# Performance work log

Hardware: AMD Instinct MI355X
Metric: run time of the kernel (lower is better)

## Reference

```python
import jax, jax.numpy as jnp
import numpy as np

GS = 8      # grid_size
NH = 8      # num_heads
DM = 256    # hidden_dim / d_model
B, W, H = 4, 256, 256


def setup_inputs() -> dict:
    key = jax.random.key(0)
    ks = jax.random.split(key, 5)
    s = 0.02
    return {
        "x": jax.random.normal(ks[0], (B, DM, W, H), dtype=jnp.float32),
        "Wq": jax.random.normal(ks[1], (DM, DM), dtype=jnp.float32) * s,
        "bq": jnp.zeros((DM,), dtype=jnp.float32),
        "Wk": jax.random.normal(ks[2], (DM, DM), dtype=jnp.float32) * s,
        "bk": jnp.zeros((DM,), dtype=jnp.float32),
        "Wv": jax.random.normal(ks[3], (DM, DM), dtype=jnp.float32) * s,
        "bv": jnp.zeros((DM,), dtype=jnp.float32),
        "Wo": jax.random.normal(ks[4], (DM, DM), dtype=jnp.float32) * s,
        "bo": jnp.zeros((DM,), dtype=jnp.float32),
    }


def reference(x, Wq, bq, Wk, bk, Wv, bv, Wo, bo):
    b, d, w, h = x.shape
    gw, gh = w // GS, h // GS
    n = gw * gh               # num grid cells
    L = GS * GS               # tokens per cell
    dh = d // NH

    # query: avg-pool each grid cell -> (b*n, 1, d)
    q = x.reshape(b, d, gw, GS, gh, GS).mean(axis=(3, 5))      # (b, d, gw, gh)
    q = q.reshape(b, d, n).transpose(0, 2, 1).reshape(b * n, 1, d)

    # K/V: per-cell patch tokens, (b*n, L, d); matches torch unfold layout
    kv = x.transpose(0, 2, 3, 1)                                # (b, w, h, d)
    kv = kv.reshape(b, gw, GS, gh, GS, d)
    kv = kv.transpose(0, 1, 3, 2, 4, 5).reshape(b * n, L, d)

    # multi-head cross-attention (standard: q/k/v/out linear + softmax)
    qp = (q @ Wq.T + bq).reshape(b * n, 1, NH, dh).transpose(0, 2, 1, 3)   # (bn, H, 1, dh)
    kp = (kv @ Wk.T + bk).reshape(b * n, L, NH, dh).transpose(0, 2, 1, 3)  # (bn, H, L, dh)
    vp = (kv @ Wv.T + bv).reshape(b * n, L, NH, dh).transpose(0, 2, 1, 3)

    scores = jnp.einsum("bhqd,bhkd->bhqk", qp, kp) / jnp.sqrt(jnp.float32(dh))
    attn = jax.nn.softmax(scores, axis=-1)                      # (bn, H, 1, L)
    ctx = jnp.einsum("bhqk,bhkd->bhqd", attn, vp)               # (bn, H, 1, dh)
    ctx = ctx.transpose(0, 2, 1, 3).reshape(b * n, 1, d)
    attn_out = ctx @ Wo.T + bo                                  # (bn, 1, d)

    out = q + attn_out
    return out.reshape(b, n, d)
```

## Files before the change

kernel.cpp:

```cpp
#include <hip/hip_runtime.h>
#include <hip/hip_bf16.h>


#define NCELL 4096

typedef float f32x4 __attribute__((ext_vector_type(4)));
typedef short s16x8 __attribute__((ext_vector_type(8)));

#define OFF_NT 0u
#define OFF_BE 262144u
#define OFF_S 1310976u
#define OFF_WQB 5505280u
#define OFF_WKB 5538048u

__device__ __forceinline__ unsigned short bfrnd(float f) {
  unsigned u = __float_as_uint(f);
  u += 0x7fffu + ((u >> 16) & 1u);
  return (unsigned short)(u >> 16);
}
__device__ __forceinline__ float bflo(unsigned u) { return __uint_as_float(u << 16); }
__device__ __forceinline__ float bfhi(unsigned u) { return __uint_as_float(u & 0xffff0000u); }

__global__ __launch_bounds__(256) void k_cvt(const float* __restrict__ Wq, const float* __restrict__ Wk,
                                             unsigned short* __restrict__ WQB, unsigned short* __restrict__ WKB) {
  const int i = blockIdx.x * 256 + threadIdx.x;
  {
    const float4 v = *reinterpret_cast<const float4*>(Wq + i * 4);
    const unsigned lo = (unsigned)bfrnd(v.x) | ((unsigned)bfrnd(v.y) << 16);
    const unsigned hi = (unsigned)bfrnd(v.z) | ((unsigned)bfrnd(v.w) << 16);
    *reinterpret_cast<uint2*>(WQB + i * 4) = make_uint2(lo, hi);
  }
  {
    const float4 v = *reinterpret_cast<const float4*>(Wk + i * 4);
    const unsigned lo = (unsigned)bfrnd(v.x) | ((unsigned)bfrnd(v.y) << 16);
    const unsigned hi = (unsigned)bfrnd(v.z) | ((unsigned)bfrnd(v.w) << 16);
    *reinterpret_cast<uint2*>(WKB + i * 4) = make_uint2(lo, hi);
  }
}

__global__ __launch_bounds__(256) void k_nt(const float* __restrict__ Wv, const float* __restrict__ Wo,
                                            unsigned short* __restrict__ NT) {
  __shared__ float wo_s[32];
  const int n = blockIdx.x >> 3, h = blockIdx.x & 7;
  const int j = threadIdx.x;
  if (threadIdx.x < 32) wo_s[threadIdx.x] = Wo[n * 256 + h * 32 + threadIdx.x];
  __syncthreads();
  float acc = 0.f;
#pragma unroll
  for (int i = 0; i < 32; ++i) acc += Wv[(h * 32 + i) * 256 + j] * wo_s[i];
  NT[(size_t)n * 2048 + h * 256 + j] = bfrnd(acc);
}

__global__ __launch_bounds__(256) void k_beff(const float* __restrict__ bo, const float* __restrict__ bv,
                                              const float* __restrict__ Wo, float* __restrict__ BE) {
  const int w = threadIdx.x >> 6, l = threadIdx.x & 63;
  const int k = blockIdx.x * 4 + w;
  float acc = 0.f;
#pragma unroll
  for (int c = 0; c < 4; ++c) acc += bv[l + 64 * c] * Wo[k * 256 + l + 64 * c];
#pragma unroll
  for (int mk = 32; mk >= 1; mk >>= 1) acc += __shfl_xor(acc, mk);
  if (l == 0) BE[k] = acc + bo[k];
}

__global__ __launch_bounds__(256, 3) void k_cell(
    const float* __restrict__ x,
    const unsigned short* __restrict__ WQB, const float* __restrict__ bq,
    const unsigned short* __restrict__ WKB, const float* __restrict__ bk,
    const float* __restrict__ BE,
    float* __restrict__ out, unsigned short* __restrict__ Sg) {
  __shared__ __align__(16) unsigned short xb[256 * 72];
  __shared__ __align__(16) float q_s[256];
  __shared__ __align__(16) float qp_s[256];
  __shared__ __align__(16) unsigned short r_bf[8 * 264];
  __shared__ __align__(16) float R1[2304];
  __shared__ float off_s[8];

  const int tid = threadIdx.x;
  const int cell = ((blockIdx.x & 7) << 9) | (blockIdx.x >> 3);
  const int b = cell >> 10, cw = (cell >> 5) & 31, ch = cell & 31;
  const float* xp = x + (size_t)b * 16777216 + (size_t)cw * 2048 + (size_t)ch * 8;

  const int i_row = (tid >> 1) & 7, half = tid & 1, d0 = tid >> 4;
  const float* tb = xp + (size_t)d0 * 65536 + i_row * 256 + half * 4;
  float4 v[16];
#pragma unroll
  for (int it = 0; it < 16; ++it)
    v[it] = *reinterpret_cast<const float4*>(tb + (size_t)it * 1048576);
  const int t0 = i_row * 8 + half * 4;
#pragma unroll
  for (int it = 0; it < 16; ++it) {
    const int d = it * 16 + d0;
    const unsigned lo = (unsigned)bfrnd(v[it].x) | ((unsigned)bfrnd(v[it].y) << 16);
    const unsigned hi = (unsigned)bfrnd(v[it].z) | ((unsigned)bfrnd(v[it].w) << 16);
    *reinterpret_cast<uint2*>(&xb[d * 72 + t0]) = make_uint2(lo, hi);
    float ps = (v[it].x + v[it].y) + (v[it].z + v[it].w);
    ps += __shfl_xor(ps, 1);
    ps += __shfl_xor(ps, 2);
    ps += __shfl_xor(ps, 4);
    ps += __shfl_xor(ps, 8);
    if ((tid & 15) == 0) q_s[d] = ps * (1.0f / 64.0f);
  }
  __syncthreads();

  out[(size_t)cell * 256 + tid] = q_s[tid] + BE[tid];

  {
    const int io = tid >> 5, jl = tid & 31;
    float qr[8];
    *reinterpret_cast<float4*>(qr) = *reinterpret_cast<const float4*>(&q_s[jl * 8]);
    *reinterpret_cast<float4*>(qr + 4) = *reinterpret_cast<const float4*>(&q_s[jl * 8 + 4]);
#pragma unroll
    for (int rb = 0; rb < 8; ++rb) {
      float acc[4];
#pragma unroll
      for (int rr = 0; rr < 4; ++rr) {
        const int i = (rb * 4 + rr) * 8 + io;
        const uint4 wv = *reinterpret_cast<const uint4*>(WQB + i * 256 + jl * 8);
        acc[rr] = bflo(wv.x) * qr[0] + bfhi(wv.x) * qr[1] + bflo(wv.y) * qr[2] + bfhi(wv.y) * qr[3] +
                  bflo(wv.z) * qr[4] + bfhi(wv.z) * qr[5] + bflo(wv.w) * qr[6] + bfhi(wv.w) * qr[7];
      }
#pragma unroll
      for (int mk = 16; mk >= 1; mk >>= 1) {
#pragma unroll
        for (int rr = 0; rr < 4; ++rr) acc[rr] += __shfl_xor(acc[rr], mk);
      }
      if (jl == 0) {
#pragma unroll
        for (int rr = 0; rr < 4; ++rr) {
          const int i = (rb * 4 + rr) * 8 + io;
          qp_s[i] = (acc[rr] + bq[i]) * 0.17677669529663689f;
        }
      }
    }
  }
  __syncthreads();

  {
    const int hw = tid >> 6;
    const int j0 = (tid & 63) * 4;
#pragma unroll
    for (int hh = 0; hh < 2; ++hh) {
      const int h = hw * 2 + hh;
      float a0 = 0.f, a1 = 0.f, a2 = 0.f, a3 = 0.f;
#pragma unroll
      for (int i = 0; i < 32; ++i) {
        const float s = qp_s[h * 32 + i];
        const uint2 wv = *reinterpret_cast<const uint2*>(WKB + (h * 32 + i) * 256 + j0);
        a0 += s * bflo(wv.x);
        a1 += s * bfhi(wv.x);
        a2 += s * bflo(wv.y);
        a3 += s * bfhi(wv.y);
      }
      const unsigned lo = (unsigned)bfrnd(a0) | ((unsigned)bfrnd(a1) << 16);
      const unsigned hi = (unsigned)bfrnd(a2) | ((unsigned)bfrnd(a3) << 16);
      *reinterpret_cast<uint2*>(&r_bf[h * 264 + j0]) = make_uint2(lo, hi);
    }
    if (tid < 8) {
      float o = 0.f;
      for (int i = 0; i < 32; ++i) o += qp_s[tid * 32 + i] * bk[tid * 32 + i];
      off_s[tid] = o;
    }
  }
  __syncthreads();

  {
    const int t = tid & 63, p = tid >> 6;
    float xr[64];
#pragma unroll
    for (int dd = 0; dd < 64; ++dd) {
      const unsigned vv = xb[(p * 64 + dd) * 72 + t];
      xr[dd] = __uint_as_float(vv << 16);
    }
#pragma unroll
    for (int h = 0; h < 8; ++h) {
      float acc = 0.f;
#pragma unroll
      for (int dc = 0; dc < 8; ++dc) {
        const uint4 rv = *reinterpret_cast<const uint4*>(&r_bf[h * 264 + p * 64 + dc * 8]);
        acc += bflo(rv.x) * xr[dc * 8 + 0] + bfhi(rv.x) * xr[dc * 8 + 1] +
               bflo(rv.y) * xr[dc * 8 + 2] + bfhi(rv.y) * xr[dc * 8 + 3] +
               bflo(rv.z) * xr[dc * 8 + 4] + bfhi(rv.z) * xr[dc * 8 + 5] +
               bflo(rv.w) * xr[dc * 8 + 6] + bfhi(rv.w) * xr[dc * 8 + 7];
      }
      R1[p * 576 + t * 9 + h] = acc;
    }
  }
  __syncthreads();

  {
    const int w = tid >> 6, t = tid & 63;
    float av[2];
#pragma unroll
    for (int hi = 0; hi < 2; ++hi) {
      const int h = w + hi * 4;
      const float vv = R1[0 * 576 + t * 9 + h] + R1[1 * 576 + t * 9 + h] +
                       R1[2 * 576 + t * 9 + h] + R1[3 * 576 + t * 9 + h] + off_s[h];
      float m = vv;
#pragma unroll
      for (int mk = 32; mk >= 1; mk >>= 1) m = fmaxf(m, __shfl_xor(m, mk));
      const float e = __expf(vv - m);
      float s = e;
#pragma unroll
      for (int mk = 32; mk >= 1; mk >>= 1) s += __shfl_xor(s, mk);
      av[hi] = e / s;
    }
    __syncthreads();
    R1[t * 12 + w] = av[0];
    R1[t * 12 + w + 4] = av[1];
  }
  __syncthreads();

  {
    const int d = tid;
    float acc[8] = {0, 0, 0, 0, 0, 0, 0, 0};
#pragma unroll
    for (int tc = 0; tc < 8; ++tc) {
      const uint4 xv = *reinterpret_cast<const uint4*>(&xb[d * 72 + tc * 8]);
      const float xf[8] = {bflo(xv.x), bfhi(xv.x), bflo(xv.y), bfhi(xv.y),
                           bflo(xv.z), bfhi(xv.z), bflo(xv.w), bfhi(xv.w)};
#pragma unroll
      for (int k = 0; k < 8; ++k) {
        const int t = tc * 8 + k;
        const float4 aA = *reinterpret_cast<const float4*>(&R1[t * 12]);
        const float4 aB = *reinterpret_cast<const float4*>(&R1[t * 12 + 4]);
        acc[0] += aA.x * xf[k]; acc[1] += aA.y * xf[k];
        acc[2] += aA.z * xf[k]; acc[3] += aA.w * xf[k];
        acc[4] += aB.x * xf[k]; acc[5] += aB.y * xf[k];
        acc[6] += aB.z * xf[k]; acc[7] += aB.w * xf[k];
      }
    }
#pragma unroll
    for (int h = 0; h < 8; ++h)
      Sg[(size_t)cell * 2048 + h * 256 + d] = bfrnd(acc[h]);
  }
}

__global__ __launch_bounds__(256, 4) void k_out(
    const unsigned short* __restrict__ Sg, const unsigned short* __restrict__ NT,
    float* __restrict__ out) {
  __shared__ __align__(16) unsigned short As[64 * 72];
  __shared__ __align__(16) unsigned short Bs[64 * 72];
  const int tid = threadIdx.x;
  const int tile = blockIdx.x >> 2, ks = blockIdx.x & 3;
  const int m0 = (tile >> 2) * 64, n0 = (tile & 3) * 64;
  const int w = tid >> 6, l = tid & 63;
  const int wm = (w & 1) * 32, wn = (w >> 1) * 32;
  const int lr = l & 15, lq = l >> 4;

  f32x4 acc[2][2];
#pragma unroll
  for (int a = 0; a < 2; ++a)
#pragma unroll
    for (int c = 0; c < 2; ++c) acc[a][c] = (f32x4){0.f, 0.f, 0.f, 0.f};

  const int srow = tid >> 2, sseg = tid & 3;
  const size_t arow = (size_t)(m0 + srow) * 2048 + sseg * 16;
  const size_t brow = (size_t)(n0 + srow) * 2048 + sseg * 16;
  const int kbase = ks * 512;

  uint4 a0v = *reinterpret_cast<const uint4*>(&Sg[arow + kbase]);
  uint4 a1v = *reinterpret_cast<const uint4*>(&Sg[arow + kbase + 8]);
  uint4 b0v = *reinterpret_cast<const uint4*>(&NT[brow + kbase]);
  uint4 b1v = *reinterpret_cast<const uint4*>(&NT[brow + kbase + 8]);

  for (int kt = 0; kt < 8; ++kt) {
    __syncthreads();
    *reinterpret_cast<uint4*>(&As[srow * 72 + sseg * 16]) = a0v;
    *reinterpret_cast<uint4*>(&As[srow * 72 + sseg * 16 + 8]) = a1v;
    *reinterpret_cast<uint4*>(&Bs[srow * 72 + sseg * 16]) = b0v;
    *reinterpret_cast<uint4*>(&Bs[srow * 72 + sseg * 16 + 8]) = b1v;
    __syncthreads();
    if (kt < 7) {
      const int kn = kbase + (kt + 1) * 64;
      a0v = *reinterpret_cast<const uint4*>(&Sg[arow + kn]);
      a1v = *reinterpret_cast<const uint4*>(&Sg[arow + kn + 8]);
      b0v = *reinterpret_cast<const uint4*>(&NT[brow + kn]);
      b1v = *reinterpret_cast<const uint4*>(&NT[brow + kn + 8]);
    }
#pragma unroll
    for (int s = 0; s < 2; ++s) {
      s16x8 af[2], bfr[2];
#pragma unroll
      for (int a = 0; a < 2; ++a)
        af[a] = *reinterpret_cast<const s16x8*>(&As[(wm + a * 16 + lr) * 72 + s * 32 + lq * 8]);
#pragma unroll
      for (int c = 0; c < 2; ++c)
        bfr[c] = *reinterpret_cast<const s16x8*>(&Bs[(wn + c * 16 + lr) * 72 + s * 32 + lq * 8]);
#pragma unroll
      for (int a = 0; a < 2; ++a)
#pragma unroll
        for (int c = 0; c < 2; ++c)
          acc[a][c] = __builtin_amdgcn_mfma_f32_16x16x32_bf16(af[a], bfr[c], acc[a][c], 0, 0, 0);
    }
  }
#pragma unroll
  for (int a = 0; a < 2; ++a) {
#pragma unroll
    for (int c = 0; c < 2; ++c) {
      const int col = n0 + wn + c * 16 + lr;
#pragma unroll
      for (int rr = 0; rr < 4; ++rr) {
        const int row = m0 + wm + a * 16 + lq * 4 + rr;
        atomicAdd(&out[(size_t)row * 256 + col], acc[a][c][rr]);
      }
    }
  }
}

extern "C" void kernel_launch(void* const* d_in, const int* in_sizes, int n_in,
                              void* d_out, int out_size, void* d_ws, size_t ws_size,
                              hipStream_t stream) {
  const float* x = (const float*)d_in[0];
  const float* Wq = (const float*)d_in[1];
  const float* bq = (const float*)d_in[2];
  const float* Wk = (const float*)d_in[3];
  const float* bk = (const float*)d_in[4];
  const float* Wv = (const float*)d_in[5];
  const float* bv = (const float*)d_in[6];
  const float* Wo = (const float*)d_in[7];
  const float* bo = (const float*)d_in[8];
  float* ws = (float*)d_ws;
  unsigned short* NT = (unsigned short*)(ws + OFF_NT);
  float* BE = ws + OFF_BE;
  unsigned short* Sg = (unsigned short*)(ws + OFF_S);
  unsigned short* WQB = (unsigned short*)(ws + OFF_WQB);
  unsigned short* WKB = (unsigned short*)(ws + OFF_WKB);
  float* out = (float*)d_out;

  hipLaunchKernelGGL(k_cvt, dim3(64), dim3(256), 0, stream, Wq, Wk, WQB, WKB);
  hipLaunchKernelGGL(k_nt, dim3(2048), dim3(256), 0, stream, Wv, Wo, NT);
  hipLaunchKernelGGL(k_beff, dim3(64), dim3(256), 0, stream, bo, bv, Wo, BE);
  hipLaunchKernelGGL(k_cell, dim3(NCELL), dim3(256), 0, stream, x, WQB, bq, WKB, bk, BE, out, Sg);
  hipLaunchKernelGGL(k_out, dim3(1024), dim3(256), 0, stream, Sg, NT, out);
}
```

Measured before the change: 687.9 us.

## Load x tiles directly into LDS as fp32 via global_load_lds

Replaces the register-staged load, bf16 conversion and shuffle-based pooling of the x tile with direct global-to-LDS loads (global_load_lds, 16 bytes per lane) into an fp32 LDS buffer. The pooled mean is then computed from LDS with rotated chunk offsets to spread bank accesses, and the later stages read fp32 directly instead of unpacking bf16. The goal is to cut register pressure and VALU conversion work on the load path. In exchange the LDS footprint roughly doubles, and occupancy is lowered from 3 to 2 blocks per CU.

```diff
diff --git a/kernel.cpp b/kernel.cpp
--- a/kernel.cpp
+++ b/kernel.cpp
@@ -20,6 +20,12 @@
 }
 __device__ __forceinline__ float bflo(unsigned u) { return __uint_as_float(u << 16); }
 __device__ __forceinline__ float bfhi(unsigned u) { return __uint_as_float(u & 0xffff0000u); }
+
+__device__ __forceinline__ void gl_lds16(const float* g, float* l) {
+  __builtin_amdgcn_global_load_lds(
+      (const __attribute__((address_space(1))) unsigned int*)g,
+      (__attribute__((address_space(3))) unsigned int*)l, 16, 0, 0);
+}
 
 __global__ __launch_bounds__(256) void k_cvt(const float* __restrict__ Wq, const float* __restrict__ Wk,
                                              unsigned short* __restrict__ WQB, unsigned short* __restrict__ WKB) {
@@ -63,13 +69,13 @@
   if (l == 0) BE[k] = acc + bo[k];
 }
 
-__global__ __launch_bounds__(256, 3) void k_cell(
+__global__ __launch_bounds__(256, 2) void k_cell(
     const float* __restrict__ x,
     const unsigned short* __restrict__ WQB, const float* __restrict__ bq,
     const unsigned short* __restrict__ WKB, const float* __restrict__ bk,
     const float* __restrict__ BE,
     float* __restrict__ out, unsigned short* __restrict__ Sg) {
-  __shared__ __align__(16) unsigned short xb[256 * 72];
+  __shared__ __align__(16) float xb[256 * 64];
   __shared__ __align__(16) float q_s[256];
   __shared__ __align__(16) float qp_s[256];
   __shared__ __align__(16) unsigned short r_bf[8 * 264];
@@ -81,29 +87,32 @@
   const int b = cell >> 10, cw = (cell >> 5) & 31, ch = cell & 31;
   const float* xp = x + (size_t)b * 16777216 + (size_t)cw * 2048 + (size_t)ch * 8;
 
-  const int i_row = (tid >> 1) & 7, half = tid & 1, d0 = tid >> 4;
-  const float* tb = xp + (size_t)d0 * 65536 + i_row * 256 + half * 4;
-  float4 v[16];
-#pragma unroll
-  for (int it = 0; it < 16; ++it)
-    v[it] = *reinterpret_cast<const float4*>(tb + (size_t)it * 1048576);
-  const int t0 = i_row * 8 + half * 4;
-#pragma unroll
-  for (int it = 0; it < 16; ++it) {
-    const int d = it * 16 + d0;
-    const unsigned lo = (unsigned)bfrnd(v[it].x) | ((unsigned)bfrnd(v[it].y) << 16);
-    const unsigned hi = (unsigned)bfrnd(v[it].z) | ((unsigned)bfrnd(v[it].w) << 16);
-    *reinterpret_cast<uint2*>(&xb[d * 72 + t0]) = make_uint2(lo, hi);
-    float ps = (v[it].x + v[it].y) + (v[it].z + v[it].w);
-    ps += __shfl_xor(ps, 1);
-    ps += __shfl_xor(ps, 2);
-    ps += __shfl_xor(ps, 4);
-    ps += __shfl_xor(ps, 8);
-    if ((tid & 15) == 0) q_s[d] = ps * (1.0f / 64.0f);
-  }
-  __syncthreads();
-
-  out[(size_t)cell * 256 + tid] = q_s[tid] + BE[tid];
+  {
+    const int w = tid >> 6, l = tid & 63;
+    const int dl = l >> 4;
+    const int m = l & 15;
+    const int i_row = m >> 1, j0 = (m & 1) * 4;
+    const float* gs0 = xp + (size_t)dl * 65536 + i_row * 256 + j0;
+#pragma unroll
+    for (int k = 0; k < 16; ++k) {
+      const int dbase = w * 64 + k * 4;
+      gl_lds16(gs0 + (size_t)dbase * 65536, &xb[dbase * 64 + l * 4]);
+    }
+  }
+  __syncthreads();
+
+  {
+    f32x4 s4 = {0.f, 0.f, 0.f, 0.f};
+#pragma unroll
+    for (int c = 0; c < 16; ++c) {
+      const int chunk = (tid + c) & 15;
+      s4 += *reinterpret_cast<const f32x4*>(&xb[tid * 64 + chunk * 4]);
+    }
+    const float qv = (s4.x + s4.y + s4.z + s4.w) * (1.0f / 64.0f);
+    q_s[tid] = qv;
+    out[(size_t)cell * 256 + tid] = qv + BE[tid];
+  }
+  __syncthreads();
 
   {
     const int io = tid >> 5, jl = tid & 31;
@@ -168,10 +177,7 @@
     const int t = tid & 63, p = tid >> 6;
     float xr[64];
 #pragma unroll
-    for (int dd = 0; dd < 64; ++dd) {
-      const unsigned vv = xb[(p * 64 + dd) * 72 + t];
-      xr[dd] = __uint_as_float(vv << 16);
-    }
+    for (int dd = 0; dd < 64; ++dd) xr[dd] = xb[(p * 64 + dd) * 64 + t];
 #pragma unroll
     for (int h = 0; h < 8; ++h) {
       float acc = 0.f;
@@ -215,19 +221,19 @@
     const int d = tid;
     float acc[8] = {0, 0, 0, 0, 0, 0, 0, 0};
 #pragma unroll
-    for (int tc = 0; tc < 8; ++tc) {
-      const uint4 xv = *reinterpret_cast<const uint4*>(&xb[d * 72 + tc * 8]);
-      const float xf[8] = {bflo(xv.x), bfhi(xv.x), bflo(xv.y), bfhi(xv.y),
-                           bflo(xv.z), bfhi(xv.z), bflo(xv.w), bfhi(xv.w)};
-#pragma unroll
-      for (int k = 0; k < 8; ++k) {
-        const int t = tc * 8 + k;
+    for (int tc = 0; tc < 16; ++tc) {
+      const int chunk = (d + tc) & 15;
+      const f32x4 xv = *reinterpret_cast<const f32x4*>(&xb[d * 64 + chunk * 4]);
+#pragma unroll
+      for (int k = 0; k < 4; ++k) {
+        const int t = chunk * 4 + k;
+        const float xf = xv[k];
         const float4 aA = *reinterpret_cast<const float4*>(&R1[t * 12]);
         const float4 aB = *reinterpret_cast<const float4*>(&R1[t * 12 + 4]);
-        acc[0] += aA.x * xf[k]; acc[1] += aA.y * xf[k];
-        acc[2] += aA.z * xf[k]; acc[3] += aA.w * xf[k];
-        acc[4] += aB.x * xf[k]; acc[5] += aB.y * xf[k];
-        acc[6] += aB.z * xf[k]; acc[7] += aB.w * xf[k];
+        acc[0] += aA.x * xf; acc[1] += aA.y * xf;
+        acc[2] += aA.z * xf; acc[3] += aA.w * xf;
+        acc[4] += aB.x * xf; acc[5] += aB.y * xf;
+        acc[6] += aB.z * xf; acc[7] += aB.w * xf;
       }
     }
 #pragma unroll
```

Result: faster. 576.4 us (-16.2%).
